# Performance work log

Measured on AMD Instinct MI355X. Metric: run time of the kernel, lower is better.

Reference implementation:

```python
import jax, jax.numpy as jnp
import numpy as np

BN_EPS = 1e-5


def setup_inputs() -> dict:
    key = jax.random.key(0)
    ks = jax.random.split(key, 8)
    B, C, N = 4, 256, 4096
    s = 1.0 / np.sqrt(C)
    return {
        "feature": jax.random.normal(ks[0], (B, C, N, 1), dtype=jnp.float32),
        "Wa": jax.random.normal(ks[1], (C, C), dtype=jnp.float32) * s,
        "ba": jnp.zeros((C,), dtype=jnp.float32),
        "Wb": jax.random.normal(ks[2], (C, C), dtype=jnp.float32) * s,
        "bb": jnp.zeros((C,), dtype=jnp.float32),
        "Wm": jax.random.normal(ks[3], (C, C), dtype=jnp.float32) * s,
        "bm": jnp.zeros((C,), dtype=jnp.float32),
        "gamma": jnp.ones((C,), dtype=jnp.float32),
        "beta": jnp.zeros((C,), dtype=jnp.float32),
        "rmean": jnp.zeros((C,), dtype=jnp.float32),
        "rvar": jnp.ones((C,), dtype=jnp.float32),
        "alpha": jnp.zeros((1,), dtype=jnp.float32),
    }


def reference(feature, Wa, ba, Wb, bb, Wm, bm, gamma, beta, rmean, rvar, alpha):
    # feature: [B, C, N, 1]; 1x1 convs are per-point linear maps over channels.
    x = feature[..., 0]  # [B, C, N]
    a = jnp.einsum('oc,bcn->bon', Wa, x) + ba[None, :, None]  # fc_a
    b = jnp.einsum('oc,bcn->bon', Wb, x) + bb[None, :, None]  # fc_b
    # att = softmax(a^T @ b) over last dim: [B, N, N]
    att = jax.nn.softmax(jnp.einsum('bcn,bcm->bnm', a, b), axis=2)
    # mlp: 1x1 conv + eval-mode BatchNorm
    m = jnp.einsum('oc,bcn->bon', Wm, x) + bm[None, :, None]
    inv = jax.lax.rsqrt(rvar + BN_EPS)
    m = (m - rmean[None, :, None]) * (inv * gamma)[None, :, None] + beta[None, :, None]
    # f = att @ m^T -> [B, N, C], back to [B, C, N]
    f = jnp.einsum('bnm,bcm->bcn', att, m)
    return feature + alpha[0] * f[..., None]
```

## Files before the change

### kernel.cpp

```cpp
#include <hip/hip_runtime.h>
#include <hip/hip_bf16.h>

typedef __bf16 bf16x8 __attribute__((ext_vector_type(8)));
typedef float f32x4 __attribute__((ext_vector_type(4)));
typedef float f32x16 __attribute__((ext_vector_type(16)));
typedef int i32x4 __attribute__((ext_vector_type(4)));
typedef int i32x8 __attribute__((ext_vector_type(8)));
typedef unsigned int u32;

#define MFMA16 __builtin_amdgcn_mfma_f32_16x16x32_bf16
#define MFMASC(a, b, c) \
  __builtin_amdgcn_mfma_scale_f32_32x32x64_f8f6f4((a), (b), (c), 0, 0, 0, 0x7F7F7F7F, 0, 0x7F7F7F7F)

#define LOG2E 1.44269504f

__device__ __forceinline__ unsigned short f2b(float f) {
  return __builtin_bit_cast(unsigned short, (__bf16)f);
}

__device__ __forceinline__ u32 pk4(float a, float b, float c, float d) {
  int v = __builtin_amdgcn_cvt_pk_fp8_f32(a, b, 0, false);
  v = __builtin_amdgcn_cvt_pk_fp8_f32(c, d, v, true);
  return (u32)v;
}

__device__ __forceinline__ void gload_lds16(const void* g, void* l) {
  __builtin_amdgcn_global_load_lds(
      (const __attribute__((address_space(1))) unsigned int*)g,
      (__attribute__((address_space(3))) unsigned int*)l, 16, 0, 0);
}

__global__ __launch_bounds__(256) void k_wconv(const float* __restrict__ Wa,
                                               const float* __restrict__ Wb,
                                               const float* __restrict__ Wm,
                                               unsigned short* __restrict__ W16) {
  const int m = blockIdx.y;
  const float* W = (m == 0) ? Wa : (m == 1) ? Wb : Wm;
  const int i = (blockIdx.x * 256 + threadIdx.x) * 8;
  float4 a = *reinterpret_cast<const float4*>(W + i);
  float4 b = *reinterpret_cast<const float4*>(W + i + 4);
  ushort4 lo, hi;
  lo.x = f2b(a.x); lo.y = f2b(a.y); lo.z = f2b(a.z); lo.w = f2b(a.w);
  hi.x = f2b(b.x); hi.y = f2b(b.y); hi.z = f2b(b.z); hi.w = f2b(b.w);
  unsigned short* dst = W16 + m * 65536 + i;
  *reinterpret_cast<ushort4*>(dst) = lo;
  *reinterpret_cast<ushort4*>(dst + 4) = hi;
}

__global__ __launch_bounds__(256) void k_proj(
    const float* __restrict__ x, const unsigned short* __restrict__ W16,
    const float* __restrict__ ba, const float* __restrict__ bb,
    const float* __restrict__ bm, const float* __restrict__ gamma,
    const float* __restrict__ beta, const float* __restrict__ rmean,
    const float* __restrict__ rvar,
    unsigned char* __restrict__ Q8, unsigned char* __restrict__ K8,
    unsigned char* __restrict__ V8) {
  __shared__ float tile[256][36];
  __shared__ __align__(16) unsigned short XT_lds[32 * 256];
  const int nt = blockIdx.x, b = blockIdx.y;
  const int n0 = nt * 32;
  const int tid = threadIdx.x, w = tid >> 6, l = tid & 63;
  const int li = l & 15, lk = l >> 4;
  {
    const int cr = tid >> 3, j4 = (tid & 7) * 4;
#pragma unroll
    for (int p = 0; p < 8; ++p) {
      int c = p * 32 + cr;
      float4 v = *reinterpret_cast<const float4*>(
          x + ((size_t)(b * 256 + c)) * 4096 + n0 + j4);
      *reinterpret_cast<float4*>(&tile[c][j4]) = v;
    }
  }
  __syncthreads();
  {
    const int n = tid & 31, cb8 = (tid >> 5) * 32;
#pragma unroll
    for (int p = 0; p < 8; ++p) {
      int c0 = cb8 + p * 4;
      ushort4 o;
      o.x = f2b(tile[c0][n]); o.y = f2b(tile[c0 + 1][n]);
      o.z = f2b(tile[c0 + 2][n]); o.w = f2b(tile[c0 + 3][n]);
      unsigned off = ((unsigned)(n * 512 + c0 * 2)) ^ (unsigned)((n & 7) << 4);
      *reinterpret_cast<ushort4*>((char*)XT_lds + off) = o;
    }
  }
  __syncthreads();
  bf16x8 af[2][8];
#pragma unroll
  for (int rs = 0; rs < 2; ++rs) {
    const int row = rs * 16 + li;
#pragma unroll
    for (int kk = 0; kk < 8; ++kk) {
      unsigned off = ((unsigned)(row * 512 + kk * 64 + lk * 16)) ^ (unsigned)((row & 7) << 4);
      af[rs][kk] = *reinterpret_cast<const bf16x8*>((const char*)XT_lds + off);
    }
  }
  const int ofb = w * 4;
  f32x4 zero = {0.f, 0.f, 0.f, 0.f};
  f32x4 acc[2][4];
  {
#pragma unroll
    for (int rs = 0; rs < 2; ++rs)
#pragma unroll
      for (int i = 0; i < 4; ++i) acc[rs][i] = zero;
#pragma unroll
    for (int kk = 0; kk < 8; ++kk)
#pragma unroll
      for (int of = 0; of < 4; ++of) {
        bf16x8 bfv = *reinterpret_cast<const bf16x8*>(
            W16 + (size_t)((ofb + of) * 16 + li) * 256 + kk * 32 + lk * 8);
        acc[0][of] = MFMA16(bfv, af[0][kk], acc[0][of], 0, 0, 0);
        acc[1][of] = MFMA16(bfv, af[1][kk], acc[1][of], 0, 0, 0);
      }
#pragma unroll
    for (int rs = 0; rs < 2; ++rs) {
      const int n = n0 + rs * 16 + li;
      unsigned char* out = Q8 + ((size_t)b * 4096 + n) * 256;
#pragma unroll
      for (int of = 0; of < 4; ++of) {
        int c0 = (ofb + of) * 16 + lk * 4;
        float4 bs = *reinterpret_cast<const float4*>(ba + c0);
        u32 v = pk4((acc[rs][of][0] + bs.x) * LOG2E, (acc[rs][of][1] + bs.y) * LOG2E,
                    (acc[rs][of][2] + bs.z) * LOG2E, (acc[rs][of][3] + bs.w) * LOG2E);
        *reinterpret_cast<u32*>(out + c0) = v;
      }
    }
  }
  {
#pragma unroll
    for (int rs = 0; rs < 2; ++rs)
#pragma unroll
      for (int i = 0; i < 4; ++i) acc[rs][i] = zero;
#pragma unroll
    for (int kk = 0; kk < 8; ++kk)
#pragma unroll
      for (int of = 0; of < 4; ++of) {
        bf16x8 bfv = *reinterpret_cast<const bf16x8*>(
            W16 + 65536 + (size_t)((ofb + of) * 16 + li) * 256 + kk * 32 + lk * 8);
        acc[0][of] = MFMA16(bfv, af[0][kk], acc[0][of], 0, 0, 0);
        acc[1][of] = MFMA16(bfv, af[1][kk], acc[1][of], 0, 0, 0);
      }
#pragma unroll
    for (int rs = 0; rs < 2; ++rs) {
      const int n = n0 + rs * 16 + li;
      unsigned char* out = K8 + ((size_t)b * 4096 + n) * 256;
#pragma unroll
      for (int of = 0; of < 4; ++of) {
        int c0 = (ofb + of) * 16 + lk * 4;
        float4 bs = *reinterpret_cast<const float4*>(bb + c0);
        u32 v = pk4(acc[rs][of][0] + bs.x, acc[rs][of][1] + bs.y,
                    acc[rs][of][2] + bs.z, acc[rs][of][3] + bs.w);
        *reinterpret_cast<u32*>(out + c0) = v;
      }
    }
  }
  {
#pragma unroll
    for (int rs = 0; rs < 2; ++rs)
#pragma unroll
      for (int i = 0; i < 4; ++i) acc[rs][i] = zero;
#pragma unroll
    for (int kk = 0; kk < 8; ++kk)
#pragma unroll
      for (int of = 0; of < 4; ++of) {
        bf16x8 bfv = *reinterpret_cast<const bf16x8*>(
            W16 + 131072 + (size_t)((ofb + of) * 16 + li) * 256 + kk * 32 + lk * 8);
        acc[0][of] = MFMA16(af[0][kk], bfv, acc[0][of], 0, 0, 0);
        acc[1][of] = MFMA16(af[1][kk], bfv, acc[1][of], 0, 0, 0);
      }
#pragma unroll
    for (int of = 0; of < 4; ++of) {
      int c = (ofb + of) * 16 + li;
      float g = rsqrtf(rvar[c] + 1e-5f) * gamma[c];
      float sh = (bm[c] - rmean[c]) * g + beta[c];
#pragma unroll
      for (int rs = 0; rs < 2; ++rs) {
        const int nn0 = n0 + rs * 16 + lk * 4;
        u32 v = pk4(acc[rs][of][0] * g + sh, acc[rs][of][1] * g + sh,
                    acc[rs][of][2] * g + sh, acc[rs][of][3] * g + sh);
        *reinterpret_cast<u32*>(
            V8 + ((size_t)b * 128 + (nn0 >> 5)) * 8192 + c * 32 + (nn0 & 31)) = v;
      }
    }
  }
}

__global__ __launch_bounds__(256, 2) void k_attn(
    const unsigned char* __restrict__ Q8, const unsigned char* __restrict__ K8,
    const unsigned char* __restrict__ V8, unsigned short* __restrict__ part,
    float* __restrict__ mpart, float* __restrict__ lpart) {
  __shared__ __align__(32) unsigned char K_lds[2][64 * 256];
  __shared__ __align__(32) unsigned char V_lds[2][2 * 8192];
  const int bid = blockIdx.x;
  const int swz = (bid & 7) * 64 + (bid >> 3);
  const int qt = swz & 31;
  const int bs = swz >> 5;
  const int b = bs >> 2, s = bs & 3;
  const int tid = threadIdx.x, w = tid >> 6, l = tid & 63;
  const int q = l & 31, hi = l >> 5;
  const int rowq = qt * 128 + w * 32 + q;
  i32x8 qf8[4];
  const unsigned char* qp = Q8 + ((size_t)b * 4096 + rowq) * 256 + hi * 32;
#pragma unroll
  for (int kk = 0; kk < 4; ++kk)
    qf8[kk] = *reinterpret_cast<const i32x8*>(qp + kk * 64);
  f32x16 acc[8];
#pragma unroll
  for (int i = 0; i < 8; ++i)
#pragma unroll
    for (int r = 0; r < 16; ++r) acc[i][r] = 0.f;
  float mr = 0.f, lr = 0.f;

  const int kbase = s * 1024;
  auto stageK = [&](int buf, int t) {
#pragma unroll
    for (int g = 0; g < 4; ++g) {
      int row = w * 16 + g * 4 + (l >> 4);
      int c16 = (l & 15) ^ ((row & 7) << 1);
      const unsigned char* src =
          K8 + ((size_t)b * 4096 + kbase + t * 64 + row) * 256 + c16 * 16;
      gload_lds16(src, &K_lds[buf][(w * 16 + g * 4) * 256]);
    }
  };
  auto stageV = [&](int buf, int t) {
    const unsigned char* base =
        V8 + ((size_t)b * 128 + (kbase >> 5) + t * 2) * 8192;
#pragma unroll
    for (int g = 0; g < 4; ++g)
      gload_lds16(base + (g * 4 + w) * 1024 + l * 16, &V_lds[buf][(g * 4 + w) * 1024]);
  };

  stageK(0, 0);
  stageV(0, 0);
  asm volatile("s_waitcnt vmcnt(0)" ::: "memory");
  __syncthreads();
  int cur = 0;
  for (int t = 0; t < 16; ++t) {
    if (t < 15) { stageK(cur ^ 1, t + 1); stageV(cur ^ 1, t + 1); }
    f32x16 S0, S1;
    float nmr = -mr;
#pragma unroll
    for (int r = 0; r < 16; ++r) { S0[r] = nmr; S1[r] = nmr; }
    __builtin_amdgcn_s_setprio(1);
#pragma unroll
    for (int kk = 0; kk < 4; ++kk) {
      int off = (((kk * 2 + hi) ^ (q & 7)) << 5);
      i32x8 kf0 = *reinterpret_cast<const i32x8*>(&K_lds[cur][q * 256 + off]);
      i32x8 kf1 = *reinterpret_cast<const i32x8*>(&K_lds[cur][(32 + q) * 256 + off]);
      S0 = MFMASC(kf0, qf8[kk], S0);
      S1 = MFMASC(kf1, qf8[kk], S1);
    }
    __builtin_amdgcn_s_setprio(0);
    float m0 = fmaxf(S0[0], S1[0]), m1 = fmaxf(S0[1], S1[1]);
    float m2 = fmaxf(S0[2], S1[2]), m3 = fmaxf(S0[3], S1[3]);
#pragma unroll
    for (int r = 4; r < 16; r += 4) {
      m0 = fmaxf(m0, fmaxf(S0[r + 0], S1[r + 0]));
      m1 = fmaxf(m1, fmaxf(S0[r + 1], S1[r + 1]));
      m2 = fmaxf(m2, fmaxf(S0[r + 2], S1[r + 2]));
      m3 = fmaxf(m3, fmaxf(S0[r + 3], S1[r + 3]));
    }
    float pmaxb = fmaxf(fmaxf(m0, m1), fmaxf(m2, m3));
    pmaxb = fmaxf(pmaxb, __shfl_xor(pmaxb, 32));
    if (!__all(pmaxb <= 8.0f)) {
      float d = fmaxf(pmaxb, 0.f);
      float sc = exp2f(-d);
      mr += d;
      lr *= sc;
#pragma unroll
      for (int cb = 0; cb < 8; ++cb)
#pragma unroll
        for (int r = 0; r < 16; ++r) acc[cb][r] *= sc;
#pragma unroll
      for (int r = 0; r < 16; ++r) { S0[r] -= d; S1[r] -= d; }
    }
#pragma unroll
    for (int r = 0; r < 16; ++r) { S0[r] = exp2f(S0[r]); S1[r] = exp2f(S1[r]); }
    float s0_ = S0[0] + S1[0], s1_ = S0[1] + S1[1];
    float s2_ = S0[2] + S1[2], s3_ = S0[3] + S1[3];
#pragma unroll
    for (int r = 4; r < 16; r += 4) {
      s0_ += S0[r + 0] + S1[r + 0];
      s1_ += S0[r + 1] + S1[r + 1];
      s2_ += S0[r + 2] + S1[r + 2];
      s3_ += S0[r + 3] + S1[r + 3];
    }
    float sum = (s0_ + s1_) + (s2_ + s3_);
    sum += __shfl_xor(sum, 32);
    lr += sum;
    u32 A0 = pk4(S0[0], S0[1], S0[2], S0[3]);
    u32 A1 = pk4(S0[4], S0[5], S0[6], S0[7]);
    u32 A2 = pk4(S0[8], S0[9], S0[10], S0[11]);
    u32 A3 = pk4(S0[12], S0[13], S0[14], S0[15]);
    u32 B0 = pk4(S1[0], S1[1], S1[2], S1[3]);
    u32 B1 = pk4(S1[4], S1[5], S1[6], S1[7]);
    u32 B2 = pk4(S1[8], S1[9], S1[10], S1[11]);
    u32 B3 = pk4(S1[12], S1[13], S1[14], S1[15]);
    asm volatile("v_permlane32_swap_b32 %0, %1" : "+v"(A0), "+v"(B0));
    asm volatile("v_permlane32_swap_b32 %0, %1" : "+v"(A1), "+v"(B1));
    asm volatile("v_permlane32_swap_b32 %0, %1" : "+v"(A2), "+v"(B2));
    asm volatile("v_permlane32_swap_b32 %0, %1" : "+v"(A3), "+v"(B3));
    i32x8 pb = (i32x8){(int)A0, (int)B0, (int)A1, (int)B1,
                       (int)A2, (int)B2, (int)A3, (int)B3};
    __builtin_amdgcn_s_setprio(1);
#pragma unroll
    for (int cb = 0; cb < 8; ++cb) {
      i32x8 vf = *reinterpret_cast<const i32x8*>(
          &V_lds[cur][hi * 8192 + (cb * 32 + q) * 32]);
      acc[cb] = MFMASC(vf, pb, acc[cb]);
    }
    __builtin_amdgcn_s_setprio(0);
    asm volatile("s_waitcnt vmcnt(0)" ::: "memory");
    __syncthreads();
    cur ^= 1;
  }
  const int sb = s * 4 + b;
  size_t pbase = ((size_t)sb * 4096 + rowq) * 256;
#pragma unroll
  for (int cb = 0; cb < 8; ++cb)
#pragma unroll
    for (int g = 0; g < 4; ++g) {
      ushort4 o;
      o.x = f2b(acc[cb][g * 4 + 0]); o.y = f2b(acc[cb][g * 4 + 1]);
      o.z = f2b(acc[cb][g * 4 + 2]); o.w = f2b(acc[cb][g * 4 + 3]);
      *reinterpret_cast<ushort4*>(&part[pbase + cb * 32 + g * 8 + hi * 4]) = o;
    }
  if (hi == 0) {
    mpart[sb * 4096 + rowq] = mr;
    lpart[sb * 4096 + rowq] = lr;
  }
}

__global__ __launch_bounds__(256) void k_comb(
    const unsigned short* __restrict__ part, const float* __restrict__ mpart,
    const float* __restrict__ lpart, const float* __restrict__ feat,
    const float* __restrict__ alpha, float* __restrict__ out) {
  __shared__ float wgt[4][32];
  __shared__ float tile[32][261];
  const int nt = blockIdx.x, b = blockIdx.y;
  const int n0 = nt * 32;
  const int tid = threadIdx.x;
  if (tid < 32) {
    int qn = n0 + tid;
    float m[4], lv[4];
#pragma unroll
    for (int s = 0; s < 4; ++s) {
      m[s] = mpart[(s * 4 + b) * 4096 + qn];
      lv[s] = lpart[(s * 4 + b) * 4096 + qn];
    }
    float M = fmaxf(fmaxf(m[0], m[1]), fmaxf(m[2], m[3]));
    float e[4], L = 0.f;
#pragma unroll
    for (int s = 0; s < 4; ++s) { e[s] = exp2f(m[s] - M); L += e[s] * lv[s]; }
    float inv = 1.0f / L;
#pragma unroll
    for (int s = 0; s < 4; ++s) wgt[s][tid] = e[s] * inv;
  }
  __syncthreads();
  const int row = tid >> 3;
  const int c0 = (tid & 7) * 32;
  float acc[32];
#pragma unroll
  for (int k = 0; k < 32; ++k) acc[k] = 0.f;
#pragma unroll
  for (int s = 0; s < 4; ++s) {
    float ww = wgt[s][row];
    const unsigned short* p = part + (((size_t)(s * 4 + b)) * 4096 + n0 + row) * 256 + c0;
#pragma unroll
    for (int ch = 0; ch < 4; ++ch) {
      bf16x8 v = *reinterpret_cast<const bf16x8*>(p + ch * 8);
#pragma unroll
      for (int j = 0; j < 8; ++j) acc[ch * 8 + j] += ww * (float)v[j];
    }
  }
#pragma unroll
  for (int k = 0; k < 32; ++k) tile[row][c0 + k] = acc[k];
  __syncthreads();
  const float av = alpha[0];
  const int j = tid & 7, cb = tid >> 3;
#pragma unroll
  for (int p = 0; p < 8; ++p) {
    int c = cb * 8 + p;
    size_t gbase = ((size_t)(b * 256 + c)) * 4096 + n0 + j * 4;
    float4 f4 = *reinterpret_cast<const float4*>(feat + gbase);
    float4 o;
    o.x = f4.x + av * tile[j * 4 + 0][c];
    o.y = f4.y + av * tile[j * 4 + 1][c];
    o.z = f4.z + av * tile[j * 4 + 2][c];
    o.w = f4.w + av * tile[j * 4 + 3][c];
    *reinterpret_cast<float4*>(out + gbase) = o;
  }
}

extern "C" void kernel_launch(void* const* d_in, const int* in_sizes, int n_in,
                              void* d_out, int out_size, void* d_ws, size_t ws_size,
                              hipStream_t stream) {
  const float* feat  = (const float*)d_in[0];
  const float* Wa    = (const float*)d_in[1];
  const float* ba    = (const float*)d_in[2];
  const float* Wb    = (const float*)d_in[3];
  const float* bb    = (const float*)d_in[4];
  const float* Wm    = (const float*)d_in[5];
  const float* bm    = (const float*)d_in[6];
  const float* gamma = (const float*)d_in[7];
  const float* beta  = (const float*)d_in[8];
  const float* rmean = (const float*)d_in[9];
  const float* rvar  = (const float*)d_in[10];
  const float* alpha = (const float*)d_in[11];
  float* out = (float*)d_out;
  char* ws = (char*)d_ws;
  unsigned char*  Q8   = (unsigned char*)(ws);
  unsigned char*  K8   = (unsigned char*)(ws + ((size_t)4 << 20));
  unsigned char*  V8   = (unsigned char*)(ws + ((size_t)8 << 20));
  unsigned short* part = (unsigned short*)(ws + ((size_t)16 << 20));
  unsigned short* W16  = (unsigned short*)(ws + ((size_t)48 << 20));
  float* mpart = (float*)(ws + ((size_t)48 << 20) + 393216);
  float* lpart = (float*)(ws + ((size_t)48 << 20) + 393216 + 262144);

  k_wconv<<<dim3(32, 3), 256, 0, stream>>>(Wa, Wb, Wm, W16);
  k_proj<<<dim3(128, 4), 256, 0, stream>>>(feat, W16, ba, bb, bm, gamma, beta,
                                           rmean, rvar, Q8, K8, V8);
  k_attn<<<dim3(512), 256, 0, stream>>>(Q8, K8, V8, part, mpart, lpart);
  k_comb<<<dim3(128, 4), 256, 0, stream>>>(part, mpart, lpart, feat, alpha, out);
}
```

Before: 118.9 us.

## Replace double-buffered K/V staging with single buffer and restore online-max softmax

Drops the LDS double buffer for K and V, so each tile is now loaded after compute with two barriers and a full wait, and no prefetch overlaps the MFMA work. It also changes the softmax to a conventional running max starting very negative, with a rescale threshold of 7 relative to the running max instead of an absolute threshold. Halving LDS use may raise occupancy, but global-load latency is now fully exposed each iteration. The exp now subtracts mr on every element.

```diff
diff --git a/kernel.cpp b/kernel.cpp
--- a/kernel.cpp
+++ b/kernel.cpp
@@ -189,8 +189,8 @@
     const unsigned char* __restrict__ Q8, const unsigned char* __restrict__ K8,
     const unsigned char* __restrict__ V8, unsigned short* __restrict__ part,
     float* __restrict__ mpart, float* __restrict__ lpart) {
-  __shared__ __align__(32) unsigned char K_lds[2][64 * 256];
-  __shared__ __align__(32) unsigned char V_lds[2][2 * 8192];
+  __shared__ __align__(32) unsigned char K_lds[64 * 256];
+  __shared__ __align__(32) unsigned char V_lds[2 * 8192];
   const int bid = blockIdx.x;
   const int swz = (bid & 7) * 64 + (bid >> 3);
   const int qt = swz & 31;
@@ -209,44 +209,41 @@
   for (int i = 0; i < 8; ++i)
 #pragma unroll
     for (int r = 0; r < 16; ++r) acc[i][r] = 0.f;
-  float mr = 0.f, lr = 0.f;
+  float mr = -3e38f, lr = 0.f;
 
   const int kbase = s * 1024;
-  auto stageK = [&](int buf, int t) {
+  auto stageK = [&](int t) {
 #pragma unroll
     for (int g = 0; g < 4; ++g) {
       int row = w * 16 + g * 4 + (l >> 4);
       int c16 = (l & 15) ^ ((row & 7) << 1);
       const unsigned char* src =
           K8 + ((size_t)b * 4096 + kbase + t * 64 + row) * 256 + c16 * 16;
-      gload_lds16(src, &K_lds[buf][(w * 16 + g * 4) * 256]);
+      gload_lds16(src, &K_lds[(w * 16 + g * 4) * 256]);
     }
   };
-  auto stageV = [&](int buf, int t) {
+  auto stageV = [&](int t) {
     const unsigned char* base =
         V8 + ((size_t)b * 128 + (kbase >> 5) + t * 2) * 8192;
 #pragma unroll
     for (int g = 0; g < 4; ++g)
-      gload_lds16(base + (g * 4 + w) * 1024 + l * 16, &V_lds[buf][(g * 4 + w) * 1024]);
+      gload_lds16(base + (g * 4 + w) * 1024 + l * 16, &V_lds[(g * 4 + w) * 1024]);
   };
 
-  stageK(0, 0);
-  stageV(0, 0);
+  stageK(0);
+  stageV(0);
   asm volatile("s_waitcnt vmcnt(0)" ::: "memory");
   __syncthreads();
-  int cur = 0;
   for (int t = 0; t < 16; ++t) {
-    if (t < 15) { stageK(cur ^ 1, t + 1); stageV(cur ^ 1, t + 1); }
     f32x16 S0, S1;
-    float nmr = -mr;
-#pragma unroll
-    for (int r = 0; r < 16; ++r) { S0[r] = nmr; S1[r] = nmr; }
+#pragma unroll
+    for (int r = 0; r < 16; ++r) { S0[r] = 0.f; S1[r] = 0.f; }
     __builtin_amdgcn_s_setprio(1);
 #pragma unroll
     for (int kk = 0; kk < 4; ++kk) {
       int off = (((kk * 2 + hi) ^ (q & 7)) << 5);
-      i32x8 kf0 = *reinterpret_cast<const i32x8*>(&K_lds[cur][q * 256 + off]);
-      i32x8 kf1 = *reinterpret_cast<const i32x8*>(&K_lds[cur][(32 + q) * 256 + off]);
+      i32x8 kf0 = *reinterpret_cast<const i32x8*>(&K_lds[q * 256 + off]);
+      i32x8 kf1 = *reinterpret_cast<const i32x8*>(&K_lds[(32 + q) * 256 + off]);
       S0 = MFMASC(kf0, qf8[kk], S0);
       S1 = MFMASC(kf1, qf8[kk], S1);
     }
@@ -260,22 +257,20 @@
       m2 = fmaxf(m2, fmaxf(S0[r + 2], S1[r + 2]));
       m3 = fmaxf(m3, fmaxf(S0[r + 3], S1[r + 3]));
     }
-    float pmaxb = fmaxf(fmaxf(m0, m1), fmaxf(m2, m3));
-    pmaxb = fmaxf(pmaxb, __shfl_xor(pmaxb, 32));
-    if (!__all(pmaxb <= 8.0f)) {
-      float d = fmaxf(pmaxb, 0.f);
-      float sc = exp2f(-d);
-      mr += d;
+    float pmax = fmaxf(fmaxf(m0, m1), fmaxf(m2, m3));
+    pmax = fmaxf(pmax, __shfl_xor(pmax, 32));
+    if (!__all(pmax - mr <= 7.0f)) {
+      float nm = fmaxf(mr, pmax);
+      float sc = exp2f(mr - nm);
+      mr = nm;
       lr *= sc;
 #pragma unroll
       for (int cb = 0; cb < 8; ++cb)
 #pragma unroll
         for (int r = 0; r < 16; ++r) acc[cb][r] *= sc;
-#pragma unroll
-      for (int r = 0; r < 16; ++r) { S0[r] -= d; S1[r] -= d; }
-    }
-#pragma unroll
-    for (int r = 0; r < 16; ++r) { S0[r] = exp2f(S0[r]); S1[r] = exp2f(S1[r]); }
+    }
+#pragma unroll
+    for (int r = 0; r < 16; ++r) { S0[r] = exp2f(S0[r] - mr); S1[r] = exp2f(S1[r] - mr); }
     float s0_ = S0[0] + S1[0], s1_ = S0[1] + S1[1];
     float s2_ = S0[2] + S1[2], s3_ = S0[3] + S1[3];
 #pragma unroll
@@ -306,13 +301,17 @@
 #pragma unroll
     for (int cb = 0; cb < 8; ++cb) {
       i32x8 vf = *reinterpret_cast<const i32x8*>(
-          &V_lds[cur][hi * 8192 + (cb * 32 + q) * 32]);
+          &V_lds[hi * 8192 + (cb * 32 + q) * 32]);
       acc[cb] = MFMASC(vf, pb, acc[cb]);
     }
     __builtin_amdgcn_s_setprio(0);
-    asm volatile("s_waitcnt vmcnt(0)" ::: "memory");
-    __syncthreads();
-    cur ^= 1;
+    if (t + 1 < 16) {
+      __syncthreads();
+      stageK(t + 1);
+      stageV(t + 1);
+      asm volatile("s_waitcnt vmcnt(0)" ::: "memory");
+      __syncthreads();
+    }
   }
   const int sb = s * 4 + b;
   size_t pbase = ((size_t)sb * 4096 + rowq) * 256;
```

New measurement: 115.7 us. 2.6% less time.
